# Performance work log

Hardware: AMD Instinct MI355X
Metric: run time of the kernel (lower is better)

## Reference

```python
import jax, jax.numpy as jnp
import numpy as np

SHIFT = 1  # module's random shift_direction, fixed to +1 for determinism
B, C, H, W_SP = 1024, 512, 7, 7


def setup_inputs() -> dict:
    key = jax.random.key(0)
    k1, k2 = jax.random.split(key)
    x = jax.random.normal(k1, (B, C, H, W_SP), dtype=jnp.float32)
    W = jax.random.normal(k2, (256, 3, 3, 512), dtype=jnp.float32)
    return {"x": x, "W": W}


def _forward(x, W):
    # unfold along H with kernel (3,1), padding (1,0):
    # patches[b,c,kh,h,w] = x_padded[b,c,h+kh,w]
    xp = jnp.pad(x, ((0, 0), (0, 0), (1, 1), (0, 0)))
    t2 = jnp.stack([xp[:, :, k:k + H, :] for k in range(3)], axis=2)  # (B,512,3,7,7)
    # split channels 512 -> (2,256), move group dim next to H
    t2 = t2.reshape(B, 2, 256, 3, H, W_SP)
    t2 = t2.transpose(0, 2, 3, 4, 1, 5)          # (B,256,3,7,2,7)
    t2 = t2.reshape(B, 256, 3, 14, W_SP)         # interleave (h,group) -> 14
    t2 = jnp.roll(t2, SHIFT, axis=3)             # shift along interleaved dim
    t2 = t2.reshape(B, 256, 3, 7, 2, W_SP).sum(axis=4)  # (B,256,3,7,7)
    t2 = t2.transpose(0, 1, 3, 2, 4)             # (B,256,7,3,7) = (m,l,n,j,w)
    # second shift + unfold along w with kernel 3, padding 1
    t3 = jnp.roll(t2, SHIFT, axis=4)
    tp = jnp.pad(t3, ((0, 0), (0, 0), (0, 0), (0, 0), (1, 1)))
    t3u = jnp.stack([tp[..., k:k + W_SP] for k in range(3)], axis=4)  # (B,256,7,3,3,7) = (m,l,n,j,k,p)
    # torch einsum 'mlnjok, ljki -> mnoi' with o = output position, k = kernel tap
    out = jnp.einsum('mlnjkp,ljki->mpni', t3u, W)  # wait: check axis order below
    # Note: torch permutes (m,c,h,j,kernel,pos)->(m,c,h,j,pos,kernel) before einsum,
    # so contraction is over (l,j,kernel) and output is (m, n=h, o=pos, i).
    out = jnp.einsum('mlnjkp,ljki->mnpi', t3u, W)  # (B,7,7,512)
    return out.transpose(0, 3, 1, 2)              # (B,512,7,7)


def reference(x, W):
    return _forward(x, W)
```

## Files before the change

### kernel.cpp

```cpp
#include <hip/hip_runtime.h>
#include <hip/hip_bf16.h>


typedef __bf16 bf16x8 __attribute__((ext_vector_type(8)));
typedef float f32x4 __attribute__((ext_vector_type(4)));
typedef unsigned int u32;

#define VT_OFFSET (4u << 20)
#define VT_BYTES  (7168ull * 7 * 768 * 2)
#define WS_NEED   (VT_OFFSET + VT_BYTES)

__device__ __forceinline__ void gload_lds16(const void* g, void* l) {
    __builtin_amdgcn_global_load_lds(
        (const __attribute__((address_space(1))) u32*)g,
        (__attribute__((address_space(3))) u32*)l, 16, 0, 0);
}

__global__ __launch_bounds__(256) void prep_wf(const float* __restrict__ Wg,
                                               __bf16* __restrict__ W2f) {
    __shared__ float ws_[96][65];
    const int kt = blockIdx.x % 24;
    const int it_ = blockIdx.x / 24;
    const int K0 = kt * 96;
    const int I0 = it_ * 64;
    const int tid = threadIdx.x;

    #pragma unroll
    for (int t = 0; t < 6; ++t) {
        const int u = t * 256 + tid;
        const int row = u >> 4;
        const int f4 = u & 15;
        const float4 v = *(const float4*)(Wg + (size_t)(K0 + row) * 512 + I0 + f4 * 4);
        ws_[row][f4 * 4 + 0] = v.x;
        ws_[row][f4 * 4 + 1] = v.y;
        ws_[row][f4 * 4 + 2] = v.z;
        ws_[row][f4 * 4 + 3] = v.w;
    }
    __syncthreads();

    #pragma unroll
    for (int t = 0; t < 3; ++t) {
        const int u = t * 256 + tid;
        const int q = u / 192;
        const int tap = (u / 64) % 3;
        const int i_loc = u & 63;
        bf16x8 o;
        #pragma unroll
        for (int e = 0; e < 8; ++e)
            o[e] = (__bf16)ws_[3 * (q * 8 + e) + tap][i_loc];
        const int i_g = I0 + i_loc;
        const int nb = i_g >> 7;
        const int r = i_g & 127;
        const int wnf = r >> 4;
        const int l15 = r & 15;
        const int unit = (((nb * 24 + kt) * 3 + tap) * 8 + wnf) * 64 + q * 16 + l15;
        *(bf16x8*)(W2f + (size_t)unit * 8) = o;
    }
}

__global__ __launch_bounds__(256) void prep_w(const float* __restrict__ Wg,
                                              __bf16* __restrict__ W2) {
    __shared__ float ws_[96][65];
    const int kt = blockIdx.x % 24;
    const int it_ = blockIdx.x / 24;
    const int K0 = kt * 96;
    const int I0 = it_ * 64;
    const int tid = threadIdx.x;

    #pragma unroll
    for (int t = 0; t < 6; ++t) {
        const int u = t * 256 + tid;
        const int row = u >> 4;
        const int f4 = u & 15;
        const float4 v = *(const float4*)(Wg + (size_t)(K0 + row) * 512 + I0 + f4 * 4);
        ws_[row][f4 * 4 + 0] = v.x;
        ws_[row][f4 * 4 + 1] = v.y;
        ws_[row][f4 * 4 + 2] = v.z;
        ws_[row][f4 * 4 + 3] = v.w;
    }
    __syncthreads();

    #pragma unroll
    for (int t = 0; t < 3; ++t) {
        const int u = t * 256 + tid;
        const int i = u / 12;
        const int rem = u - i * 12;
        const int tap = rem >> 2;
        const int q = rem & 3;
        bf16x8 o;
        #pragma unroll
        for (int e = 0; e < 8; ++e)
            o[e] = (__bf16)ws_[3 * (q * 8 + e) + tap][i];
        *(bf16x8*)(W2 + (size_t)(I0 + i) * 2304 + tap * 768 + 32 * kt + q * 8) = o;
    }
}

__global__ __launch_bounds__(256) void prep_v(const float* __restrict__ x,
                                              __bf16* __restrict__ Vt) {
    __shared__ float xs[256 * 49];
    const int b = blockIdx.x >> 1;
    const int g = blockIdx.x & 1;
    const int tid = threadIdx.x;

    {
        const float4* src0 = (const float4*)(x + ((size_t)b * 512 + g * 128) * 49);
        const float4* src1 = (const float4*)(x + ((size_t)b * 512 + 256 + g * 128) * 49);
        float4* dst0 = (float4*)xs;
        float4* dst1 = (float4*)(xs + 128 * 49);
        #pragma unroll
        for (int it = 0; it < 7; ++it) {
            const int q = it * 256 + tid;
            if (q < 1568) dst0[q] = src0[q];
        }
        #pragma unroll
        for (int it = 0; it < 7; ++it) {
            const int q = it * 256 + tid;
            if (q < 1568) dst1[q] = src1[q];
        }
    }
    __syncthreads();

    for (int h = 0; h < 7; ++h) {
        const int hm = (h + 6) % 7;
        for (int it = 0; it < 2; ++it) {
            const int u = it * 256 + tid;
            if (u < 336) {
                const int r = u / 48;
                const int k = u - r * 48;
                const int w = (r + 6) % 7;
                bf16x8 vv;
                #pragma unroll
                for (int e = 0; e < 8; ++e) {
                    const int c = k * 8 + e;
                    const int l = c / 3;
                    const int j = c - 3 * l;
                    const int r1 = h + j - 1;
                    const int r2 = hm + j - 1;
                    float v = 0.f;
                    if (r1 >= 0 && r1 < 7) v += xs[l * 49 + r1 * 7 + w];
                    if (r2 >= 0 && r2 < 7) v += xs[(128 + l) * 49 + r2 * 7 + w];
                    vv[e] = (__bf16)v;
                }
                *(bf16x8*)(Vt + (size_t)((b * 7 + h) * 7 + r) * 768 + g * 384 + k * 8) = vv;
            }
        }
    }
}

__global__ __launch_bounds__(256, 2) void gemm_vt(const __bf16* __restrict__ Vt,
                                                  const __bf16* __restrict__ W2f,
                                                  float* __restrict__ out) {
    __shared__ __align__(1024) char L[14464];

    const int tid = threadIdx.x;
    const int g0 = blockIdx.x;
    const int nb = (g0 >> 3) & 3;
    const int mb = ((g0 >> 5) << 3) | (g0 & 7);

    if (tid < 32) {
        const int off = (tid < 16) ? 7168 + tid * 4 : 14400 + (tid - 16) * 4;
        *(int*)(L + off) = 0;
    }

    int tsrc[2]; bool tok[2];
    #pragma unroll
    for (int it = 0; it < 2; ++it) {
        const int u = it * 256 + tid;
        tok[it] = (u < 448);
        const int bh = u / 28;
        const int rem = u - bh * 28;
        const int ct = rem >> 2;
        const int qs = rem & 3;
        const int q = qs ^ (ct & 3);
        tsrc[it] = ((mb * 16 + bh) * 7 + ct) * 1536 + q * 16;
    }

    const int lane = tid & 63;
    const int wave = tid >> 6;
    const int wm = wave >> 1;
    const int wn = wave & 1;
    const int ln15 = lane & 15;
    const int gq = lane >> 4;

    int boff[4];
    #pragma unroll
    for (int nf = 0; nf < 4; ++nf)
        boff[nf] = nb * 589824 + (wn * 4 + nf) * 1024 + lane * 16;

    int afoff[3][4];
    #pragma unroll
    for (int tap = 0; tap < 3; ++tap) {
        #pragma unroll
        for (int mf = 0; mf < 4; ++mf) {
            const int bh_l = wm * 8 + mf * 2 + (ln15 >> 3);
            const int p = ln15 & 7;
            const int ct = p + tap - 1;
            afoff[tap][mf] = (ct >= 0 && ct <= 6)
                ? bh_l * 448 + ct * 64 + ((gq ^ (ct & 3)) * 16)
                : 7168;
        }
    }

    f32x4 acc[4][4];
    #pragma unroll
    for (int a = 0; a < 4; ++a)
        #pragma unroll
        for (int bq = 0; bq < 4; ++bq) acc[a][bq] = (f32x4){0.f, 0.f, 0.f, 0.f};

    const char* VtB = (const char*)Vt;
    const char* W2fB = (const char*)W2f;

    {
        const char* vb = VtB;
        if (tok[0]) gload_lds16(vb + tsrc[0], L + tid * 16);
        if (tok[1]) gload_lds16(vb + tsrc[1], L + 4096 + tid * 16);
    }
    __syncthreads();

    for (int chunk = 0; chunk < 24; ++chunk) {
        const int cur = chunk & 1;
        if (chunk < 23) {
            const char* vb = VtB + (chunk + 1) * 64;
            char* td = L + (cur ^ 1) * 7232;
            if (tok[0]) gload_lds16(vb + tsrc[0], td + tid * 16);
            if (tok[1]) gload_lds16(vb + tsrc[1], td + 4096 + tid * 16);
        }

        const char* wb = W2fB + chunk * 24576;
        bf16x8 bfr[3][4];
        #pragma unroll
        for (int tap = 0; tap < 3; ++tap)
            #pragma unroll
            for (int nf = 0; nf < 4; ++nf)
                bfr[tap][nf] = *(const bf16x8*)(wb + tap * 8192 + boff[nf]);

        const char* Tb = L + cur * 7232;
        #pragma unroll
        for (int tap = 0; tap < 3; ++tap) {
            bf16x8 af[4];
            #pragma unroll
            for (int mf = 0; mf < 4; ++mf)
                af[mf] = *(const bf16x8*)(Tb + afoff[tap][mf]);
            #pragma unroll
            for (int mf = 0; mf < 4; ++mf)
                #pragma unroll
                for (int nf = 0; nf < 4; ++nf)
                    acc[mf][nf] = __builtin_amdgcn_mfma_f32_16x16x32_bf16(
                        af[mf], bfr[tap][nf], acc[mf][nf], 0, 0, 0);
        }

        __syncthreads();
    }

    #pragma unroll
    for (int mf = 0; mf < 4; ++mf) {
        #pragma unroll
        for (int r = 0; r < 4; ++r) {
            const int mrow = gq * 4 + r;
            const int Mg_l = wm * 64 + mf * 16 + mrow;
            const int p = Mg_l & 7;
            if (p == 7) continue;
            const int bh_l = Mg_l >> 3;
            const int bhg = mb * 16 + bh_l;
            const int b = bhg / 7;
            const int h = bhg - 7 * b;
            #pragma unroll
            for (int nf = 0; nf < 4; ++nf) {
                const int i = nb * 128 + wn * 64 + nf * 16 + ln15;
                out[(((size_t)b * 512 + i) * 7 + h) * 7 + p] = acc[mf][nf][r];
            }
        }
    }
}

__global__ __launch_bounds__(256) void gemm_shift(const float* __restrict__ x,
                                                  const __bf16* __restrict__ W2,
                                                  float* __restrict__ out) {
    __shared__ __bf16 T[16 * 10 * 40];
    __shared__ __bf16 Bt[128 * 104];

    const int tid = threadIdx.x;
    const int mb = blockIdx.x >> 2;
    const int nb = blockIdx.x & 3;
    const int i0 = nb * 128;

    const int cl  = tid & 31;
    const int bh0 = tid >> 5;
    const int bhg0 = mb * 16 + bh0;
    const int bhg1 = bhg0 + 8;
    const int b0 = bhg0 / 7, h0 = bhg0 - 7 * b0;
    const int b1 = bhg1 / 7, h1 = bhg1 - 7 * b1;
    const int hm0 = (h0 + 6) % 7, hm1 = (h1 + 6) % 7;

    for (int q = tid; q < 16 * 10 * 40 / 2; q += 256) ((int*)T)[q] = 0;

    const int lane = tid & 63;
    const int wave = tid >> 6;
    const int wm = wave >> 1;
    const int wn = wave & 1;
    const int ln15 = lane & 15;
    const int gq = lane >> 4;

    f32x4 acc[4][4];
    #pragma unroll
    for (int a = 0; a < 4; ++a)
        #pragma unroll
        for (int bq = 0; bq < 4; ++bq) acc[a][bq] = (f32x4){0.f, 0.f, 0.f, 0.f};

    __syncthreads();

    for (int chunk = 0; chunk < 24; ++chunk) {
        const int cg = chunk * 32 + cl;
        const int l = cg / 3;
        const int j = cg - 3 * l;
        {
            const int r1 = h0 + j - 1, r2 = hm0 + j - 1;
            float v[7] = {0.f, 0.f, 0.f, 0.f, 0.f, 0.f, 0.f};
            if (r1 >= 0 && r1 < 7) {
                const float* p1 = x + (((size_t)b0 * 512 + l) * 7 + r1) * 7;
                #pragma unroll
                for (int w = 0; w < 7; ++w) v[w] += p1[w];
            }
            if (r2 >= 0 && r2 < 7) {
                const float* p2 = x + (((size_t)b0 * 512 + 256 + l) * 7 + r2) * 7;
                #pragma unroll
                for (int w = 0; w < 7; ++w) v[w] += p2[w];
            }
            #pragma unroll
            for (int w = 0; w < 7; ++w)
                T[bh0 * 400 + ((w + 1) % 7 + 1) * 40 + cl] = (__bf16)v[w];
        }
        {
            const int r1 = h1 + j - 1, r2 = hm1 + j - 1;
            float v[7] = {0.f, 0.f, 0.f, 0.f, 0.f, 0.f, 0.f};
            if (r1 >= 0 && r1 < 7) {
                const float* p1 = x + (((size_t)b1 * 512 + l) * 7 + r1) * 7;
                #pragma unroll
                for (int w = 0; w < 7; ++w) v[w] += p1[w];
            }
            if (r2 >= 0 && r2 < 7) {
                const float* p2 = x + (((size_t)b1 * 512 + 256 + l) * 7 + r2) * 7;
                #pragma unroll
                for (int w = 0; w < 7; ++w) v[w] += p2[w];
            }
            #pragma unroll
            for (int w = 0; w < 7; ++w)
                T[(bh0 + 8) * 400 + ((w + 1) % 7 + 1) * 40 + cl] = (__bf16)v[w];
        }

        #pragma unroll
        for (int it = 0; it < 6; ++it) {
            const int u = it * 256 + tid;
            const int tap = u >> 9;
            const int rem = u & 511;
            const int n = rem >> 2;
            const int q = rem & 3;
            const float4 val = *(const float4*)(W2 + (size_t)(i0 + n) * 2304 +
                                                tap * 768 + chunk * 32 + q * 8);
            *(float4*)(&Bt[n * 104 + tap * 32 + q * 8]) = val;
        }

        __syncthreads();

        #pragma unroll
        for (int tap = 0; tap < 3; ++tap) {
            bf16x8 af[4], bfr[4];
            #pragma unroll
            for (int mf = 0; mf < 4; ++mf) {
                const int bh_l = wm * 8 + mf * 2 + (ln15 >> 3);
                const int p = ln15 & 7;
                af[mf] = *(const bf16x8*)(&T[(bh_l * 10 + p + tap) * 40 + gq * 8]);
            }
            #pragma unroll
            for (int nf = 0; nf < 4; ++nf) {
                const int n_l = wn * 64 + nf * 16 + ln15;
                bfr[nf] = *(const bf16x8*)(&Bt[n_l * 104 + tap * 32 + gq * 8]);
            }
            #pragma unroll
            for (int mf = 0; mf < 4; ++mf)
                #pragma unroll
                for (int nf = 0; nf < 4; ++nf)
                    acc[mf][nf] = __builtin_amdgcn_mfma_f32_16x16x32_bf16(
                        af[mf], bfr[nf], acc[mf][nf], 0, 0, 0);
        }

        __syncthreads();
    }

    #pragma unroll
    for (int mf = 0; mf < 4; ++mf) {
        #pragma unroll
        for (int r = 0; r < 4; ++r) {
            const int mrow = gq * 4 + r;
            const int Mg_l = wm * 64 + mf * 16 + mrow;
            const int p = Mg_l & 7;
            if (p == 7) continue;
            const int bh_l = Mg_l >> 3;
            const int bhg = mb * 16 + bh_l;
            const int b = bhg / 7;
            const int h = bhg - 7 * b;
            #pragma unroll
            for (int nf = 0; nf < 4; ++nf) {
                const int i = i0 + wn * 64 + nf * 16 + ln15;
                out[(((size_t)b * 512 + i) * 7 + h) * 7 + p] = acc[mf][nf][r];
            }
        }
    }
}

extern "C" void kernel_launch(void* const* d_in, const int* in_sizes, int n_in,
                              void* d_out, int out_size, void* d_ws, size_t ws_size,
                              hipStream_t stream) {
    const float* x  = (const float*)d_in[0];
    const float* Wg = (const float*)d_in[1];
    float* out = (float*)d_out;

    if (ws_size >= WS_NEED) {
        __bf16* W2f = (__bf16*)d_ws;
        __bf16* Vt = (__bf16*)((char*)d_ws + VT_OFFSET);
        prep_wf<<<dim3(192), dim3(256), 0, stream>>>(Wg, W2f);
        prep_v<<<dim3(2048), dim3(256), 0, stream>>>(x, Vt);
        gemm_vt<<<dim3(448 * 4), dim3(256), 0, stream>>>(Vt, W2f, out);
    } else {
        __bf16* W2 = (__bf16*)d_ws;
        prep_w<<<dim3(192), dim3(256), 0, stream>>>(Wg, W2);
        gemm_shift<<<dim3(448 * 4), dim3(256), 0, stream>>>(x, W2, out);
    }
}
```

Baseline: 367.7 us.

## Restructure gemm_vt: stage weights in LDS, fold taps into N, shift-add epilogue

The GEMM kernel now treats the three W-direction taps as extra output columns (N=384 per block: 128 channels × 3 taps) and computes a 112×384 tile per block with a 7×6 MFMA fragment grid per wave. Weights are repacked into a swizzled layout and double-buffered into LDS with direct global-to-LDS loads instead of per-wave global register loads. The tap contributions are combined afterwards through an LDS slab with shifted accumulation, which also gives coalesced output writes. This trades much more LDS (about 63 KB) and a larger accumulator footprint, which may reduce occupancy, for fewer redundant A loads and no padding rows.

```diff
diff --git a/kernel.cpp b/kernel.cpp
--- a/kernel.cpp
+++ b/kernel.cpp
@@ -16,8 +16,8 @@
         (__attribute__((address_space(3))) u32*)l, 16, 0, 0);
 }
 
-__global__ __launch_bounds__(256) void prep_wf(const float* __restrict__ Wg,
-                                               __bf16* __restrict__ W2f) {
+__global__ __launch_bounds__(256) void prep_wn(const float* __restrict__ Wg,
+                                               __bf16* __restrict__ W2n) {
     __shared__ float ws_[96][65];
     const int kt = blockIdx.x % 24;
     const int it_ = blockIdx.x / 24;
@@ -43,18 +43,16 @@
         const int u = t * 256 + tid;
         const int q = u / 192;
         const int tap = (u / 64) % 3;
-        const int i_loc = u & 63;
+        const int i64 = u & 63;
         bf16x8 o;
         #pragma unroll
         for (int e = 0; e < 8; ++e)
-            o[e] = (__bf16)ws_[3 * (q * 8 + e) + tap][i_loc];
-        const int i_g = I0 + i_loc;
+            o[e] = (__bf16)ws_[3 * (q * 8 + e) + tap][i64];
+        const int i_g = I0 + i64;
         const int nb = i_g >> 7;
-        const int r = i_g & 127;
-        const int wnf = r >> 4;
-        const int l15 = r & 15;
-        const int unit = (((nb * 24 + kt) * 3 + tap) * 8 + wnf) * 64 + q * 16 + l15;
-        *(bf16x8*)(W2f + (size_t)unit * 8) = o;
+        const int i_loc = i_g & 127;
+        const int v = ((nb * 24 + kt) * 384 + tap * 128 + i_loc) * 4 + q;
+        *(bf16x8*)(W2n + (size_t)v * 8) = o;
     }
 }
 
@@ -148,32 +146,176 @@
 }
 
 __global__ __launch_bounds__(256, 2) void gemm_vt(const __bf16* __restrict__ Vt,
-                                                  const __bf16* __restrict__ W2f,
+                                                  const __bf16* __restrict__ W2n,
                                                   float* __restrict__ out) {
-    __shared__ __align__(1024) char L[14464];
+    __shared__ __align__(1024) char L[64512];
 
     const int tid = threadIdx.x;
     const int g0 = blockIdx.x;
     const int nb = (g0 >> 3) & 3;
-    const int mb = ((g0 >> 5) << 3) | (g0 & 7);
-
-    if (tid < 32) {
-        const int off = (tid < 16) ? 7168 + tid * 4 : 14400 + (tid - 16) * 4;
-        *(int*)(L + off) = 0;
-    }
-
-    int tsrc[2]; bool tok[2];
-    #pragma unroll
-    for (int it = 0; it < 2; ++it) {
-        const int u = it * 256 + tid;
-        tok[it] = (u < 448);
-        const int bh = u / 28;
-        const int rem = u - bh * 28;
-        const int ct = rem >> 2;
-        const int qs = rem & 3;
-        const int q = qs ^ (ct & 3);
-        tsrc[it] = ((mb * 16 + bh) * 7 + ct) * 1536 + q * 16;
-    }
+    const int Mb = ((g0 >> 5) << 3) | (g0 & 7);
+
+    const int lane = tid & 63;
+    const int wave = tid >> 6;
+    const int wn = wave;
+    const int ln15 = lane & 15;
+    const int gq = lane >> 4;
+
+    int asrc0, asrc1;
+    {
+        const int u0 = tid;
+        const int r0 = u0 >> 2, q0 = (u0 & 3) ^ ((r0 >> 1) & 3);
+        asrc0 = (Mb * 112 + r0) * 1536 + q0 * 16;
+        const int u1 = 256 + tid;
+        const int r1 = u1 >> 2, q1 = (u1 & 3) ^ ((r1 >> 1) & 3);
+        asrc1 = (tid < 192) ? (Mb * 112 + r1) * 1536 + q1 * 16 : lane * 16;
+    }
+    int bsrc[6];
+    #pragma unroll
+    for (int it = 0; it < 6; ++it) {
+        const int s = it * 256 + tid;
+        const int col = s >> 2;
+        const int q = (s & 3) ^ ((col >> 1) & 3);
+        bsrc[it] = (col * 4 + q) * 16;
+    }
+
+    int afoff[7], bfoff[6];
+    #pragma unroll
+    for (int mf = 0; mf < 7; ++mf) {
+        const int row = mf * 16 + ln15;
+        afoff[mf] = row * 64 + ((gq ^ ((row >> 1) & 3)) * 16);
+    }
+    #pragma unroll
+    for (int nf = 0; nf < 6; ++nf) {
+        const int col = wn * 96 + nf * 16 + ln15;
+        bfoff[nf] = col * 64 + ((gq ^ ((col >> 1) & 3)) * 16);
+    }
+
+    f32x4 acc[7][6];
+    #pragma unroll
+    for (int a = 0; a < 7; ++a)
+        #pragma unroll
+        for (int bq = 0; bq < 6; ++bq) acc[a][bq] = (f32x4){0.f, 0.f, 0.f, 0.f};
+
+    const char* VtB = (const char*)Vt;
+    const char* WnB = (const char*)W2n + nb * 589824;
+
+    auto stage = [&](int ck, int buf) {
+        const char* vb = VtB + ck * 64;
+        char* ad = L + buf * 7168;
+        gload_lds16(vb + asrc0, ad + tid * 16);
+        if (tid < 192) gload_lds16(vb + asrc1, ad + 4096 + tid * 16);
+        else           gload_lds16(VtB + asrc1, L + 63488 + (tid - 192) * 16);
+        const char* wb = WnB + ck * 24576;
+        char* bd = L + 14336 + buf * 24576;
+        #pragma unroll
+        for (int it = 0; it < 6; ++it)
+            gload_lds16(wb + bsrc[it], bd + it * 4096 + tid * 16);
+    };
+
+    stage(0, 0);
+    __syncthreads();
+
+    for (int chunk = 0; chunk < 24; ++chunk) {
+        const int cur = chunk & 1;
+        if (chunk < 23) stage(chunk + 1, cur ^ 1);
+
+        const char* Ab = L + cur * 7168;
+        const char* Bb = L + 14336 + cur * 24576;
+        bf16x8 af[7], bfr[6];
+        #pragma unroll
+        for (int mf = 0; mf < 7; ++mf)
+            af[mf] = *(const bf16x8*)(Ab + afoff[mf]);
+        #pragma unroll
+        for (int nf = 0; nf < 6; ++nf)
+            bfr[nf] = *(const bf16x8*)(Bb + bfoff[nf]);
+        #pragma unroll
+        for (int mf = 0; mf < 7; ++mf)
+            #pragma unroll
+            for (int nf = 0; nf < 6; ++nf)
+                acc[mf][nf] = __builtin_amdgcn_mfma_f32_16x16x32_bf16(
+                    af[mf], bfr[nf], acc[mf][nf], 0, 0, 0);
+
+        __syncthreads();
+    }
+
+    float* slab = (float*)L;
+    #pragma unroll
+    for (int nf = 0; nf < 6; ++nf) {
+        const int cbase = wn * 96 + nf * 16;
+        if ((cbase >> 7) != 1) continue;
+        const int i_loc = (cbase & 127) + ln15;
+        #pragma unroll
+        for (int mf = 0; mf < 7; ++mf)
+            #pragma unroll
+            for (int r = 0; r < 4; ++r) {
+                const int ml = mf * 16 + gq * 4 + r;
+                const int bh = ml / 7, t = ml - 7 * bh;
+                slab[(bh * 7 + t) * 129 + i_loc] = acc[mf][nf][r];
+            }
+    }
+    __syncthreads();
+    #pragma unroll
+    for (int nf = 0; nf < 6; ++nf) {
+        const int cbase = wn * 96 + nf * 16;
+        if ((cbase >> 7) != 0) continue;
+        const int i_loc = cbase + ln15;
+        #pragma unroll
+        for (int mf = 0; mf < 7; ++mf)
+            #pragma unroll
+            for (int r = 0; r < 4; ++r) {
+                const int ml = mf * 16 + gq * 4 + r;
+                const int bh = ml / 7, t = ml - 7 * bh;
+                if (t < 6) slab[(bh * 7 + t + 1) * 129 + i_loc] += acc[mf][nf][r];
+            }
+    }
+    __syncthreads();
+    #pragma unroll
+    for (int nf = 0; nf < 6; ++nf) {
+        const int cbase = wn * 96 + nf * 16;
+        if ((cbase >> 7) != 2) continue;
+        const int i_loc = (cbase & 127) + ln15;
+        #pragma unroll
+        for (int mf = 0; mf < 7; ++mf)
+            #pragma unroll
+            for (int r = 0; r < 4; ++r) {
+                const int ml = mf * 16 + gq * 4 + r;
+                const int bh = ml / 7, t = ml - 7 * bh;
+                if (t > 0) slab[(bh * 7 + t - 1) * 129 + i_loc] += acc[mf][nf][r];
+            }
+    }
+    __syncthreads();
+    for (int z = tid; z < 2048; z += 256) {
+        const int bh_loc = z >> 7, i_loc = z & 127;
+        const int bhg = Mb * 16 + bh_loc;
+        const int b = bhg / 7, h = bhg - 7 * b;
+        float* op = out + (((size_t)b * 512 + nb * 128 + i_loc) * 7 + h) * 7;
+        const float* sp = slab + bh_loc * 903 + i_loc;
+        #pragma unroll
+        for (int p = 0; p < 7; ++p) op[p] = sp[p * 129];
+    }
+}
+
+__global__ __launch_bounds__(256) void gemm_shift(const float* __restrict__ x,
+                                                  const __bf16* __restrict__ W2,
+                                                  float* __restrict__ out) {
+    __shared__ __bf16 T[16 * 10 * 40];
+    __shared__ __bf16 Bt[128 * 104];
+
+    const int tid = threadIdx.x;
+    const int mb = blockIdx.x >> 2;
+    const int nb = blockIdx.x & 3;
+    const int i0 = nb * 128;
+
+    const int cl  = tid & 31;
+    const int bh0 = tid >> 5;
+    const int bhg0 = mb * 16 + bh0;
+    const int bhg1 = bhg0 + 8;
+    const int b0 = bhg0 / 7, h0 = bhg0 - 7 * b0;
+    const int b1 = bhg1 / 7, h1 = bhg1 - 7 * b1;
+    const int hm0 = (h0 + 6) % 7, hm1 = (h1 + 6) % 7;
+
+    for (int q = tid; q < 16 * 10 * 40 / 2; q += 256) ((int*)T)[q] = 0;
 
     const int lane = tid & 63;
     const int wave = tid >> 6;
@@ -182,71 +324,87 @@
     const int ln15 = lane & 15;
     const int gq = lane >> 4;
 
-    int boff[4];
-    #pragma unroll
-    for (int nf = 0; nf < 4; ++nf)
-        boff[nf] = nb * 589824 + (wn * 4 + nf) * 1024 + lane * 16;
-
-    int afoff[3][4];
-    #pragma unroll
-    for (int tap = 0; tap < 3; ++tap) {
-        #pragma unroll
-        for (int mf = 0; mf < 4; ++mf) {
-            const int bh_l = wm * 8 + mf * 2 + (ln15 >> 3);
-            const int p = ln15 & 7;
-            const int ct = p + tap - 1;
-            afoff[tap][mf] = (ct >= 0 && ct <= 6)
-                ? bh_l * 448 + ct * 64 + ((gq ^ (ct & 3)) * 16)
-                : 7168;
-        }
-    }
-
     f32x4 acc[4][4];
     #pragma unroll
     for (int a = 0; a < 4; ++a)
         #pragma unroll
         for (int bq = 0; bq < 4; ++bq) acc[a][bq] = (f32x4){0.f, 0.f, 0.f, 0.f};
 
-    const char* VtB = (const char*)Vt;
-    const char* W2fB = (const char*)W2f;
-
-    {
-        const char* vb = VtB;
-        if (tok[0]) gload_lds16(vb + tsrc[0], L + tid * 16);
-        if (tok[1]) gload_lds16(vb + tsrc[1], L + 4096 + tid * 16);
-    }
     __syncthreads();
 
     for (int chunk = 0; chunk < 24; ++chunk) {
-        const int cur = chunk & 1;
-        if (chunk < 23) {
-            const char* vb = VtB + (chunk + 1) * 64;
-            char* td = L + (cur ^ 1) * 7232;
-            if (tok[0]) gload_lds16(vb + tsrc[0], td + tid * 16);
-            if (tok[1]) gload_lds16(vb + tsrc[1], td + 4096 + tid * 16);
-        }
-
-        const char* wb = W2fB + chunk * 24576;
-        bf16x8 bfr[3][4];
-        #pragma unroll
-        for (int tap = 0; tap < 3; ++tap)
-            #pragma unroll
-            for (int nf = 0; nf < 4; ++nf)
-                bfr[tap][nf] = *(const bf16x8*)(wb + tap * 8192 + boff[nf]);
-
-        const char* Tb = L + cur * 7232;
+        const int cg = chunk * 32 + cl;
+        const int l = cg / 3;
+        const int j = cg - 3 * l;
+        {
+            const int r1 = h0 + j - 1, r2 = hm0 + j - 1;
+            float v[7] = {0.f, 0.f, 0.f, 0.f, 0.f, 0.f, 0.f};
+            if (r1 >= 0 && r1 < 7) {
+                const float* p1 = x + (((size_t)b0 * 512 + l) * 7 + r1) * 7;
+                #pragma unroll
+                for (int w = 0; w < 7; ++w) v[w] += p1[w];
+            }
+            if (r2 >= 0 && r2 < 7) {
+                const float* p2 = x + (((size_t)b0 * 512 + 256 + l) * 7 + r2) * 7;
+                #pragma unroll
+                for (int w = 0; w < 7; ++w) v[w] += p2[w];
+            }
+            #pragma unroll
+            for (int w = 0; w < 7; ++w)
+                T[bh0 * 400 + ((w + 1) % 7 + 1) * 40 + cl] = (__bf16)v[w];
+        }
+        {
+            const int r1 = h1 + j - 1, r2 = hm1 + j - 1;
+            float v[7] = {0.f, 0.f, 0.f, 0.f, 0.f, 0.f, 0.f};
+            if (r1 >= 0 && r1 < 7) {
+                const float* p1 = x + (((size_t)b1 * 512 + l) * 7 + r1) * 7;
+                #pragma unroll
+                for (int w = 0; w < 7; ++w) v[w] += p1[w];
+            }
+            if (r2 >= 0 && r2 < 7) {
+                const float* p2 = x + (((size_t)b1 * 512 + 256 + l) * 7 + r2) * 7;
+                #pragma unroll
+                for (int w = 0; w < 7; ++w) v[w] += p2[w];
+            }
+            #pragma unroll
+            for (int w = 0; w < 7; ++w)
+                T[(bh0 + 8) * 400 + ((w + 1) % 7 + 1) * 40 + cl] = (__bf16)v[w];
+        }
+
+        #pragma unroll
+        for (int it = 0; it < 6; ++it) {
+            const int u = it * 256 + tid;
+            const int tap = u >> 9;
+            const int rem = u & 511;
+            const int n = rem >> 2;
+            const int q = rem & 3;
+            const float4 val = *(const float4*)(W2 + (size_t)(i0 + n) * 2304 +
+                                                tap * 768 + chunk * 32 + q * 8);
+            *(float4*)(&Bt[n * 104 + tap * 32 + q * 8]) = val;
+        }
+
+        __syncthreads();
+
         #pragma unroll
         for (int tap = 0; tap < 3; ++tap) {
-            bf16x8 af[4];
-            #pragma unroll
-            for (int mf = 0; mf < 4; ++mf)
-                af[mf] = *(const bf16x8*)(Tb + afoff[tap][mf]);
+            bf16x8 af[4], bfr[4];
+            #pragma unroll
+            for (int mf = 0; mf < 4; ++mf) {
+                const int bh_l = wm * 8 + mf * 2 + (ln15 >> 3);
+                const int p = ln15 & 7;
+                af[mf] = *(const bf16x8*)(&T[(bh_l * 10 + p + tap) * 40 + gq * 8]);
+            }
+            #pragma unroll
+            for (int nf = 0; nf < 4; ++nf) {
+                const int n_l = wn * 64 + nf * 16 + ln15;
+                bfr[nf] = *(const bf16x8*)(&Bt[n_l * 104 + tap * 32 + gq * 8]);
+            }
             #pragma unroll
             for (int mf = 0; mf < 4; ++mf)
                 #pragma unroll
                 for (int nf = 0; nf < 4; ++nf)
                     acc[mf][nf] = __builtin_amdgcn_mfma_f32_16x16x32_bf16(
-                        af[mf], bfr[tap][nf], acc[mf][nf], 0, 0, 0);
+                        af[mf], bfr[nf], acc[mf][nf], 0, 0, 0);
         }
 
         __syncthreads();
@@ -266,141 +424,6 @@
             const int h = bhg - 7 * b;
             #pragma unroll
             for (int nf = 0; nf < 4; ++nf) {
-                const int i = nb * 128 + wn * 64 + nf * 16 + ln15;
-                out[(((size_t)b * 512 + i) * 7 + h) * 7 + p] = acc[mf][nf][r];
-            }
-        }
-    }
-}
-
-__global__ __launch_bounds__(256) void gemm_shift(const float* __restrict__ x,
-                                                  const __bf16* __restrict__ W2,
-                                                  float* __restrict__ out) {
-    __shared__ __bf16 T[16 * 10 * 40];
-    __shared__ __bf16 Bt[128 * 104];
-
-    const int tid = threadIdx.x;
-    const int mb = blockIdx.x >> 2;
-    const int nb = blockIdx.x & 3;
-    const int i0 = nb * 128;
-
-    const int cl  = tid & 31;
-    const int bh0 = tid >> 5;
-    const int bhg0 = mb * 16 + bh0;
-    const int bhg1 = bhg0 + 8;
-    const int b0 = bhg0 / 7, h0 = bhg0 - 7 * b0;
-    const int b1 = bhg1 / 7, h1 = bhg1 - 7 * b1;
-    const int hm0 = (h0 + 6) % 7, hm1 = (h1 + 6) % 7;
-
-    for (int q = tid; q < 16 * 10 * 40 / 2; q += 256) ((int*)T)[q] = 0;
-
-    const int lane = tid & 63;
-    const int wave = tid >> 6;
-    const int wm = wave >> 1;
-    const int wn = wave & 1;
-    const int ln15 = lane & 15;
-    const int gq = lane >> 4;
-
-    f32x4 acc[4][4];
-    #pragma unroll
-    for (int a = 0; a < 4; ++a)
-        #pragma unroll
-        for (int bq = 0; bq < 4; ++bq) acc[a][bq] = (f32x4){0.f, 0.f, 0.f, 0.f};
-
-    __syncthreads();
-
-    for (int chunk = 0; chunk < 24; ++chunk) {
-        const int cg = chunk * 32 + cl;
-        const int l = cg / 3;
-        const int j = cg - 3 * l;
-        {
-            const int r1 = h0 + j - 1, r2 = hm0 + j - 1;
-            float v[7] = {0.f, 0.f, 0.f, 0.f, 0.f, 0.f, 0.f};
-            if (r1 >= 0 && r1 < 7) {
-                const float* p1 = x + (((size_t)b0 * 512 + l) * 7 + r1) * 7;
-                #pragma unroll
-                for (int w = 0; w < 7; ++w) v[w] += p1[w];
-            }
-            if (r2 >= 0 && r2 < 7) {
-                const float* p2 = x + (((size_t)b0 * 512 + 256 + l) * 7 + r2) * 7;
-                #pragma unroll
-                for (int w = 0; w < 7; ++w) v[w] += p2[w];
-            }
-            #pragma unroll
-            for (int w = 0; w < 7; ++w)
-                T[bh0 * 400 + ((w + 1) % 7 + 1) * 40 + cl] = (__bf16)v[w];
-        }
-        {
-            const int r1 = h1 + j - 1, r2 = hm1 + j - 1;
-            float v[7] = {0.f, 0.f, 0.f, 0.f, 0.f, 0.f, 0.f};
-            if (r1 >= 0 && r1 < 7) {
-                const float* p1 = x + (((size_t)b1 * 512 + l) * 7 + r1) * 7;
-                #pragma unroll
-                for (int w = 0; w < 7; ++w) v[w] += p1[w];
-            }
-            if (r2 >= 0 && r2 < 7) {
-                const float* p2 = x + (((size_t)b1 * 512 + 256 + l) * 7 + r2) * 7;
-                #pragma unroll
-                for (int w = 0; w < 7; ++w) v[w] += p2[w];
-            }
-            #pragma unroll
-            for (int w = 0; w < 7; ++w)
-                T[(bh0 + 8) * 400 + ((w + 1) % 7 + 1) * 40 + cl] = (__bf16)v[w];
-        }
-
-        #pragma unroll
-        for (int it = 0; it < 6; ++it) {
-            const int u = it * 256 + tid;
-            const int tap = u >> 9;
-            const int rem = u & 511;
-            const int n = rem >> 2;
-            const int q = rem & 3;
-            const float4 val = *(const float4*)(W2 + (size_t)(i0 + n) * 2304 +
-                                                tap * 768 + chunk * 32 + q * 8);
-            *(float4*)(&Bt[n * 104 + tap * 32 + q * 8]) = val;
-        }
-
-        __syncthreads();
-
-        #pragma unroll
-        for (int tap = 0; tap < 3; ++tap) {
-            bf16x8 af[4], bfr[4];
-            #pragma unroll
-            for (int mf = 0; mf < 4; ++mf) {
-                const int bh_l = wm * 8 + mf * 2 + (ln15 >> 3);
-                const int p = ln15 & 7;
-                af[mf] = *(const bf16x8*)(&T[(bh_l * 10 + p + tap) * 40 + gq * 8]);
-            }
-            #pragma unroll
-            for (int nf = 0; nf < 4; ++nf) {
-                const int n_l = wn * 64 + nf * 16 + ln15;
-                bfr[nf] = *(const bf16x8*)(&Bt[n_l * 104 + tap * 32 + gq * 8]);
-            }
-            #pragma unroll
-            for (int mf = 0; mf < 4; ++mf)
-                #pragma unroll
-                for (int nf = 0; nf < 4; ++nf)
-                    acc[mf][nf] = __builtin_amdgcn_mfma_f32_16x16x32_bf16(
-                        af[mf], bfr[nf], acc[mf][nf], 0, 0, 0);
-        }
-
-        __syncthreads();
-    }
-
-    #pragma unroll
-    for (int mf = 0; mf < 4; ++mf) {
-        #pragma unroll
-        for (int r = 0; r < 4; ++r) {
-            const int mrow = gq * 4 + r;
-            const int Mg_l = wm * 64 + mf * 16 + mrow;
-            const int p = Mg_l & 7;
-            if (p == 7) continue;
-            const int bh_l = Mg_l >> 3;
-            const int bhg = mb * 16 + bh_l;
-            const int b = bhg / 7;
-            const int h = bhg - 7 * b;
-            #pragma unroll
-            for (int nf = 0; nf < 4; ++nf) {
                 const int i = i0 + wn * 64 + nf * 16 + ln15;
                 out[(((size_t)b * 512 + i) * 7 + h) * 7 + p] = acc[mf][nf][r];
             }
@@ -416,11 +439,11 @@
     float* out = (float*)d_out;
 
     if (ws_size >= WS_NEED) {
-        __bf16* W2f = (__bf16*)d_ws;
+        __bf16* W2n = (__bf16*)d_ws;
         __bf16* Vt = (__bf16*)((char*)d_ws + VT_OFFSET);
-        prep_wf<<<dim3(192), dim3(256), 0, stream>>>(Wg, W2f);
+        prep_wn<<<dim3(192), dim3(256), 0, stream>>>(Wg, W2n);
         prep_v<<<dim3(2048), dim3(256), 0, stream>>>(x, Vt);
-        gemm_vt<<<dim3(448 * 4), dim3(256), 0, stream>>>(Vt, W2f, out);
+        gemm_vt<<<dim3(448 * 4), dim3(256), 0, stream>>>(Vt, W2n, out);
     } else {
         __bf16* W2 = (__bf16*)d_ws;
         prep_w<<<dim3(192), dim3(256), 0, stream>>>(Wg, W2);
```

Result: slower. 429.9 us (+16.9%).
